# Kernel optimization log

Hardware: AMD Instinct MI355X
Metric: run time of the kernel (lower is better)

Reference implementation:

```python
import jax, jax.numpy as jnp
import numpy as np

B, NN, D, H, L, E, NC = 512, 64, 128, 4, 2, 262144, 8
N = B * NN
HD = D // H


def _mlp(x, W1, b1, W2, b2):
    return jax.nn.relu(x @ W1 + b1) @ W2 + b2


def setup_inputs() -> dict:
    key = jax.random.key(0)
    ks = iter(jax.random.split(key, 64))
    w = lambda shape, s=0.02: jax.random.normal(next(ks), shape, dtype=jnp.float32) * s
    inp = {
        'node_features': jax.random.randint(next(ks), (N,), 0, NC, dtype=jnp.int32),
        'edge_index': jax.random.randint(next(ks), (2, E), 0, N, dtype=jnp.int32),
        'ptr': jnp.arange(B + 1, dtype=jnp.int32) * NN,
        'node_emb_table': w((NC, D), 1.0),
        'edge_emb': jnp.clip(jax.random.normal(next(ks), (1, D), dtype=jnp.float32), -2.0, 2.0),
        'eW1': w((L, 3 * D, D)), 'eb1': jnp.zeros((L, D)), 'eW2': w((L, D, D)), 'eb2': jnp.zeros((L, D)),
        'nW1': w((L, 3 * D, D)), 'nb1': jnp.zeros((L, D)), 'nW2': w((L, D, D)), 'nb2': jnp.zeros((L, D)),
        'gW1': w((L, 3 * D, D)), 'gb1': jnp.zeros((L, D)), 'gW2': w((L, D, D)), 'gb2': jnp.zeros((L, D)),
        'projW': w((D, 3 * D)), 'projb': jnp.zeros((3 * D,)),
        'Wq': w((D, D)), 'Wk': w((D, D)), 'Wv': w((D, D)),
        'bq': jnp.zeros((D,)), 'bk': jnp.zeros((D,)), 'bv': jnp.zeros((D,)),
        'outW': w((D, D)), 'outb': jnp.zeros((D,)),
        'sW1': w((D, D)), 'sb1': jnp.zeros((D,)), 'sW2': w((D, D)), 'sb2': jnp.zeros((D,)),
        'rW1': w((D, D)), 'rb1': jnp.zeros((D,)), 'rW2': w((D, D)), 'rb2': jnp.zeros((D,)),
        'stW1': w((D, D)), 'stb1': jnp.zeros((D,)), 'stW2': w((D, 1)), 'stb2': jnp.zeros((1,)),
        'temperature': jnp.float32(1.0),
    }
    return inp


def reference(node_features, edge_index, ptr, node_emb_table, edge_emb,
              eW1, eb1, eW2, eb2, nW1, nb1, nW2, nb2, gW1, gb1, gW2, gb2,
              projW, projb, Wq, Wk, Wv, bq, bk, bv, outW, outb,
              sW1, sb1, sW2, sb2, rW1, rb1, rW2, rb2,
              stW1, stb1, stW2, stb2, temperature):
    n_graphs = ptr.shape[0] - 1                       # static
    batch_idx = jnp.repeat(jnp.arange(n_graphs), NN)  # uniform graphs of NN nodes
    node_embs = node_emb_table[node_features]         # [N, D]
    edge_embs = jnp.broadcast_to(edge_emb, (edge_index.shape[1], D))  # [E, D]
    g = jnp.zeros((n_graphs, D), node_embs.dtype)
    src, dst = edge_index[0], edge_index[1]
    for l in range(L):
        ein = jnp.concatenate([node_embs[src], node_embs[dst], edge_embs], -1)  # [E, 3D]
        edge_embs = edge_embs + _mlp(ein, eW1[l], eb1[l], eW2[l], eb2[l])
        node_aggr = jax.ops.segment_sum(edge_embs, dst, num_segments=N)         # [N, D]
        nin = jnp.concatenate([node_embs, node_aggr, g[batch_idx]], -1)
        node_embs = node_embs + _mlp(nin, nW1[l], nb1[l], nW2[l], nb2[l])
        eg = jax.ops.segment_sum(node_aggr, batch_idx, num_segments=n_graphs)
        ng = jax.ops.segment_sum(node_embs, batch_idx, num_segments=n_graphs)
        g = g + _mlp(jnp.concatenate([ng, eg, g], -1), gW1[l], gb1[l], gW2[l], gb2[l])
    # projection + self-attention over the NN nodes of each graph
    x = node_embs.reshape(n_graphs, NN, D) @ projW + projb   # [B, NN, 3D]
    q, k, v = jnp.split(x, 3, axis=-1)
    qh = (q @ Wq + bq).reshape(n_graphs, NN, H, HD)
    kh = (k @ Wk + bk).reshape(n_graphs, NN, H, HD)
    vh = (v @ Wv + bv).reshape(n_graphs, NN, H, HD)
    scores = jnp.einsum('bqhd,bkhd->bhqk', qh, kh) / jnp.sqrt(jnp.float32(HD))
    attn = jax.nn.softmax(scores, axis=-1)
    ctx = jnp.einsum('bhqk,bkhd->bqhd', attn, vh).reshape(n_graphs, NN, D)
    a = ctx @ outW + outb
    senders = _mlp(a, sW1, sb1, sW2, sb2)
    receivers = _mlp(a, rW1, rb1, rW2, rb2)
    edge_actions = jnp.einsum('bqd,bkd->bqk', senders, receivers).reshape(n_graphs, NN * NN)
    edge_actions = edge_actions / jax.nn.softplus(temperature)
    stop = _mlp(g, stW1, stb1, stW2, stb2)[:, 0]
    at = jnp.full((n_graphs, 3), -jnp.inf, dtype=edge_actions.dtype)
    at = at.at[:, 1].set(jax.nn.log_sigmoid(-stop))   # ADD_EDGE
    at = at.at[:, 2].set(jax.nn.log_sigmoid(stop))    # EXIT
    return (at, edge_actions)
```

## Files before the change

kernel.cpp:

```cpp
#include <hip/hip_runtime.h>
#include <hip/hip_bf16.h>
#include <cstdint>
#include <cstddef>

#define D_   128
#define NN_  64
#define B_   512
#define N_   32768
#define E_   262144

typedef float4 f4;
typedef _Float16 h16;
typedef __attribute__((ext_vector_type(8))) _Float16 h16x8;
typedef __attribute__((ext_vector_type(4))) float f32x4;

__device__ __forceinline__ f4 ld4(const float* p) { return *(const f4*)p; }
__device__ __forceinline__ void st4(float* p, f4 v) { *(f4*)p = v; }

__device__ __forceinline__ int swz(int row, int slot) {
  return row * 128 + ((slot ^ (row & 7)) << 3);
}
__device__ __forceinline__ h16x8 pk8(f4 a, f4 b) {
  h16x8 v;
  v[0]=(h16)a.x; v[1]=(h16)a.y; v[2]=(h16)a.z; v[3]=(h16)a.w;
  v[4]=(h16)b.x; v[5]=(h16)b.y; v[6]=(h16)b.z; v[7]=(h16)b.w;
  return v;
}
#define MFMA16(a,b,c) __builtin_amdgcn_mfma_f32_16x16x32_f16((a),(b),(c),0,0,0)

__device__ __forceinline__ void stage_a32(const float* __restrict__ A, h16* A_s, int r0, int tid) {
  int r = tid >> 2, q = tid & 3;
  const float* Ar = A + (size_t)(r0 + r) * 128 + q * 32;
#pragma unroll
  for (int i = 0; i < 4; ++i)
    *(h16x8*)&A_s[swz(r, q * 4 + i)] = pk8(ld4(Ar + i * 8), ld4(Ar + i * 8 + 4));
}
__device__ __forceinline__ void stage_a16(const h16* __restrict__ A, h16* A_s, int r0, int tid) {
  int r = tid >> 2, q = tid & 3;
  const h16* Ar = A + (size_t)(r0 + r) * 128 + q * 32;
#pragma unroll
  for (int i = 0; i < 4; ++i)
    *(h16x8*)&A_s[swz(r, q * 4 + i)] = *(const h16x8*)(Ar + i * 8);
}
__device__ __forceinline__ void bfrag_g(const h16* __restrict__ Bt, int n0, int lq, int lr, h16x8 bf[2][4]) {
#pragma unroll
  for (int nf = 0; nf < 2; ++nf) {
    const h16* row = Bt + (size_t)(n0 + nf * 16 + lr) * 128 + lq * 8;
#pragma unroll
    for (int ks = 0; ks < 4; ++ks)
      bf[nf][ks] = *(const h16x8*)(row + ks * 32);
  }
}
__device__ __forceinline__ void mfma8(const h16* A_s, h16x8 bf[2][4], f32x4 acc[4][2], int lq, int lr) {
#pragma unroll
  for (int mf = 0; mf < 4; ++mf)
#pragma unroll
    for (int ks = 0; ks < 4; ++ks) {
      h16x8 af = *(h16x8*)&A_s[swz(mf * 16 + lr, ks * 4 + lq)];
      acc[mf][0] = MFMA16(af, bf[0][ks], acc[mf][0]);
      acc[mf][1] = MFMA16(af, bf[1][ks], acc[mf][1]);
    }
}
__device__ __forceinline__ void zacc(f32x4 acc[4][2]) {
#pragma unroll
  for (int mf = 0; mf < 4; ++mf) { acc[mf][0] = (f32x4)0.f; acc[mf][1] = (f32x4)0.f; }
}

__global__ __launch_bounds__(256)
void k_embed(const int* __restrict__ nf, const float* __restrict__ tab, float* __restrict__ out) {
  int idx = blockIdx.x * 256 + threadIdx.x;
  int row = idx >> 5, q = idx & 31;
  st4(out + (size_t)row * D_ + q * 4, ld4(tab + (size_t)nf[row] * D_ + q * 4));
}

__global__ __launch_bounds__(256)
void k_zero_cnt(int* __restrict__ cnt) { cnt[blockIdx.x * 256 + threadIdx.x] = 0; }

__global__ __launch_bounds__(256)
void k_hist(const int* __restrict__ dst, int* __restrict__ cnt) {
  atomicAdd(&cnt[dst[blockIdx.x * 256 + threadIdx.x]], 1);
}

__global__ __launch_bounds__(256)
void k_scan(const int* __restrict__ cnt, int* __restrict__ base, int* __restrict__ cursor) {
  __shared__ int sums[256];
  __shared__ int offs[256];
  const int t = threadIdx.x;
  const int start = t * 128;
  int s = 0;
  for (int i = 0; i < 128; ++i) s += cnt[start + i];
  sums[t] = s;
  __syncthreads();
  if (t == 0) { int acc = 0; for (int i = 0; i < 256; ++i) { offs[i] = acc; acc += sums[i]; } }
  __syncthreads();
  int off = offs[t];
  for (int i = 0; i < 128; ++i) { base[start + i] = off; cursor[start + i] = off; off += cnt[start + i]; }
  if (t == 255) base[N_] = off;
}

__global__ __launch_bounds__(256)
void k_scatter(const int* __restrict__ dst, int* __restrict__ cursor, int* __restrict__ eid) {
  int e = blockIdx.x * 256 + threadIdx.x;
  int p = atomicAdd(&cursor[dst[e]], 1);
  eid[p] = e;
}

__global__ __launch_bounds__(256)
void k_aggr(const h16* __restrict__ edgeb, const int* __restrict__ csrB,
            float* __restrict__ aggr) {
  const int node = blockIdx.x * 4 + (threadIdx.x >> 6);
  const int d2 = (threadIdx.x & 63) * 2;
  const int b0 = csrB[node], b1 = csrB[node + 1];
  float s0 = 0.f, s1 = 0.f;
  for (int i = b0; i < b1; ++i) {
    const h16* p = edgeb + (size_t)i * 128 + d2;
    s0 += (float)p[0]; s1 += (float)p[1];
  }
  aggr[(size_t)node * 128 + d2 + 0] = s0;
  aggr[(size_t)node * 128 + d2 + 1] = s1;
}

struct TP { const float* p[32]; };
__global__ __launch_bounds__(256)
void k_w2t(TP tp, h16* __restrict__ dst) {
  __shared__ h16 w_s[128][132];
  const float* S = tp.p[blockIdx.x];
  h16* Dd = dst + (size_t)blockIdx.x * 16384;
  const int t = threadIdx.x, r = t >> 1, hf = t & 1;
  for (int i = 0; i < 64; i += 4) {
    f4 x = ld4(S + r * 128 + hf * 64 + i);
    w_s[r][hf*64+i+0] = (h16)x.x; w_s[r][hf*64+i+1] = (h16)x.y;
    w_s[r][hf*64+i+2] = (h16)x.z; w_s[r][hf*64+i+3] = (h16)x.w;
  }
  __syncthreads();
  for (int i8 = 0; i8 < 64; i8 += 8) {
    h16x8 v;
#pragma unroll
    for (int j = 0; j < 8; ++j) v[j] = w_s[hf*64 + i8 + j][r];
    *(h16x8*)(Dd + (size_t)r * 128 + hf * 64 + i8) = v;
  }
}

__global__ __launch_bounds__(256, 2)
void k_weff(const float* __restrict__ projW, const h16* __restrict__ wt_qkv,
            h16* __restrict__ wout) {
  __shared__ h16 A_s[64 * 128];
  const int i = blockIdx.x >> 1, half = blockIdx.x & 1;
  const int r0 = half * 64;
  const int tid = threadIdx.x;
  const int lane = tid & 63, w = tid >> 6;
  const int n0 = w * 32, lq = lane >> 4, lr = lane & 15;
  stage_a16(wt_qkv + (size_t)i * 16384, A_s, r0, tid);
  __syncthreads();
  h16x8 bf[2][4];
#pragma unroll
  for (int nf = 0; nf < 2; ++nf) {
    const int r = n0 + nf * 16 + lr;
    const float* prow = projW + (size_t)r * 384 + i * 128 + lq * 8;
#pragma unroll
    for (int ks = 0; ks < 4; ++ks)
      bf[nf][ks] = pk8(ld4(prow + ks * 32), ld4(prow + ks * 32 + 4));
  }
  f32x4 acc[4][2];
  zacc(acc);
  mfma8(A_s, bf, acc, lq, lr);
  h16* Wo = wout + (size_t)i * 16384;
#pragma unroll
  for (int nf = 0; nf < 2; ++nf) {
    const int r = n0 + nf * 16 + lr;
#pragma unroll
    for (int mf = 0; mf < 4; ++mf)
#pragma unroll
      for (int reg = 0; reg < 4; ++reg)
        Wo[(size_t)(r0 + mf * 16 + lq * 4 + reg) * 128 + r] = (h16)acc[mf][nf][reg];
  }
}

__global__ __launch_bounds__(256, 2)
void k_gemm3o(const float* __restrict__ A,
              const h16* __restrict__ B1, const h16* __restrict__ B2,
              const h16* __restrict__ B3,
              const float* __restrict__ bias,
              h16* __restrict__ O1, h16* __restrict__ O2, h16* __restrict__ O3) {
  __shared__ h16 A_s[64 * 128];
  const int tid = threadIdx.x;
  const int r0 = blockIdx.x * 64;
  const int lane = tid & 63, w = tid >> 6;
  const int n0 = w * 32, lq = lane >> 4, lr = lane & 15;
  stage_a32(A, A_s, r0, tid);
  __syncthreads();
  const h16* Bs[3] = {B1, B2, B3};
  h16*       Os[3] = {O1, O2, O3};
#pragma unroll
  for (int o = 0; o < 3; ++o) {
    if (!Bs[o]) break;
    h16x8 bf[2][4];
    f32x4 acc[4][2];
    bfrag_g(Bs[o], n0, lq, lr, bf);
    zacc(acc);
    mfma8(A_s, bf, acc, lq, lr);
#pragma unroll
    for (int nf = 0; nf < 2; ++nf) {
      const int col = n0 + nf * 16 + lr;
      const float bv = bias ? bias[o * 128 + col] : 0.f;
#pragma unroll
      for (int mf = 0; mf < 4; ++mf)
#pragma unroll
        for (int reg = 0; reg < 4; ++reg)
          Os[o][(size_t)(r0 + mf * 16 + lq * 4 + reg) * 128 + col] = (h16)(acc[mf][nf][reg] + bv);
    }
  }
}

__global__ __launch_bounds__(256, 2)
void k_mlp2(const float* __restrict__ A1, const float* __restrict__ A2,
            const float* __restrict__ A3,
            const h16* __restrict__ B1a, const h16* __restrict__ B1b,
            const h16* __restrict__ B1c,
            const float* __restrict__ bias1,
            const h16* __restrict__ B2, const float* __restrict__ bias2,
            const float* __restrict__ addC,
            float* __restrict__ C) {
  __shared__ h16 A_s[64 * 128];
  const int tid = threadIdx.x;
  const int r0 = blockIdx.x * 64;
  const int lane = tid & 63, w = tid >> 6;
  const int n0 = w * 32, lq = lane >> 4, lr = lane & 15;
  h16x8 bf[2][4];
  f32x4 acc[4][2];
  zacc(acc);
  stage_a32(A1, A_s, r0, tid);
  __syncthreads();
  bfrag_g(B1a, n0, lq, lr, bf);
  mfma8(A_s, bf, acc, lq, lr);
  if (A2) {
    __syncthreads();
    stage_a32(A2, A_s, r0, tid);
    __syncthreads();
    bfrag_g(B1b, n0, lq, lr, bf);
    mfma8(A_s, bf, acc, lq, lr);
  }
  if (A3) {
    __syncthreads();
    stage_a32(A3, A_s, r0, tid);
    __syncthreads();
    bfrag_g(B1c, n0, lq, lr, bf);
    mfma8(A_s, bf, acc, lq, lr);
  }
  __syncthreads();
#pragma unroll
  for (int nf = 0; nf < 2; ++nf) {
    const int col = n0 + nf * 16 + lr;
    const float b1v = bias1 ? bias1[col] : 0.f;
#pragma unroll
    for (int mf = 0; mf < 4; ++mf)
#pragma unroll
      for (int reg = 0; reg < 4; ++reg) {
        const int row = mf * 16 + lq * 4 + reg;
        A_s[swz(row, col >> 3) + (col & 7)] = (h16)fmaxf(acc[mf][nf][reg] + b1v, 0.f);
      }
  }
  __syncthreads();
  bfrag_g(B2, n0, lq, lr, bf);
  zacc(acc);
  mfma8(A_s, bf, acc, lq, lr);
#pragma unroll
  for (int nf = 0; nf < 2; ++nf) {
    const int col = n0 + nf * 16 + lr;
    const float b2v = bias2 ? bias2[col] : 0.f;
#pragma unroll
    for (int mf = 0; mf < 4; ++mf)
#pragma unroll
      for (int reg = 0; reg < 4; ++reg) {
        const int row = r0 + mf * 16 + lq * 4 + reg;
        float x = acc[mf][nf][reg] + b2v;
        if (addC) x += addC[(size_t)row * 128 + col];
        C[(size_t)row * 128 + col] = x;
      }
  }
}

__global__ __launch_bounds__(256, 2)
void k_nodemlp(float* __restrict__ node, const float* __restrict__ aggr,
               const float* __restrict__ gbuf,
               const h16* __restrict__ B1a, const h16* __restrict__ B1b,
               const float* __restrict__ nW1c, const float* __restrict__ nb1,
               const h16* __restrict__ B2, const float* __restrict__ nb2,
               float* __restrict__ ngb, float* __restrict__ egb) {
  __shared__ h16 A_s[64 * 128];
  __shared__ float gt_s[2][128];
  __shared__ float eg_s[2][128];
  const int tid = threadIdx.x, g = blockIdx.x, r0 = g * 64;
  const int lane = tid & 63, w = tid >> 6;
  const int n0 = w * 32, lq = lane >> 4, lr = lane & 15;
  h16x8 bf[2][4];
  f32x4 acc[4][2];
  zacc(acc);
  stage_a32(node, A_s, r0, tid);
  __syncthreads();
  bfrag_g(B1a, n0, lq, lr, bf);
  mfma8(A_s, bf, acc, lq, lr);
  {
    const int col = tid & 127, half = tid >> 7;
    float s = 0.f;
    const float* gb = gbuf + (size_t)g * 128;
    for (int j = half * 64; j < half * 64 + 64; ++j)
      s += gb[j] * nW1c[(size_t)j * 128 + col];
    gt_s[half][col] = s;
  }
  __syncthreads();
  stage_a32(aggr, A_s, r0, tid);
  __syncthreads();
  bfrag_g(B1b, n0, lq, lr, bf);
  mfma8(A_s, bf, acc, lq, lr);
  {
    const int col = tid & 127, half = tid >> 7;
    float s = 0.f;
    for (int r = half * 32; r < half * 32 + 32; ++r)
      s += aggr[((size_t)r0 + r) * 128 + col];
    eg_s[half][col] = s;
  }
  __syncthreads();
#pragma unroll
  for (int nf = 0; nf < 2; ++nf) {
    const int col = n0 + nf * 16 + lr;
    const float gt = gt_s[0][col] + gt_s[1][col] + nb1[col];
#pragma unroll
    for (int mf = 0; mf < 4; ++mf)
#pragma unroll
      for (int reg = 0; reg < 4; ++reg) {
        const int row = mf * 16 + lq * 4 + reg;
        A_s[swz(row, col >> 3) + (col & 7)] = (h16)fmaxf(acc[mf][nf][reg] + gt, 0.f);
      }
  }
  if (tid < 128) egb[(size_t)g * 128 + tid] = eg_s[0][tid] + eg_s[1][tid];
  __syncthreads();
  bfrag_g(B2, n0, lq, lr, bf);
  zacc(acc);
  mfma8(A_s, bf, acc, lq, lr);
#pragma unroll
  for (int nf = 0; nf < 2; ++nf) {
    const int col = n0 + nf * 16 + lr;
    const float b2v = nb2[col];
    float cs = 0.f;
#pragma unroll
    for (int mf = 0; mf < 4; ++mf)
#pragma unroll
      for (int reg = 0; reg < 4; ++reg) {
        const int row = r0 + mf * 16 + lq * 4 + reg;
        float x = acc[mf][nf][reg] + b2v + node[(size_t)row * 128 + col];
        node[(size_t)row * 128 + col] = x;
        cs += x;
      }
    cs += __shfl_xor(cs, 16);
    cs += __shfl_xor(cs, 32);
    if (lq == 0) ngb[(size_t)g * 128 + col] = cs;
  }
}

__global__ __launch_bounds__(256, 2)
void k_mlp2d(const float* __restrict__ A,
             const h16* __restrict__ B1a, const float* __restrict__ b1a,
             const h16* __restrict__ B2a, const float* __restrict__ b2a, h16* __restrict__ O1,
             const h16* __restrict__ B1b, const float* __restrict__ b1b,
             const h16* __restrict__ B2b, const float* __restrict__ b2b, h16* __restrict__ O2) {
  __shared__ h16 A_s[64 * 128];
  __shared__ h16 H_s[64 * 128];
  const int tid = threadIdx.x, r0 = blockIdx.x * 64;
  const int lane = tid & 63, w = tid >> 6;
  const int n0 = w * 32, lq = lane >> 4, lr = lane & 15;
  stage_a32(A, A_s, r0, tid);
  __syncthreads();
  const h16* W1[2] = {B1a, B1b};
  const h16* W2[2] = {B2a, B2b};
  const float* bb1[2] = {b1a, b1b};
  const float* bb2[2] = {b2a, b2b};
  h16* OO[2] = {O1, O2};
#pragma unroll
  for (int c = 0; c < 2; ++c) {
    h16x8 bf[2][4];
    f32x4 acc[4][2];
    bfrag_g(W1[c], n0, lq, lr, bf);
    zacc(acc);
    mfma8(A_s, bf, acc, lq, lr);
#pragma unroll
    for (int nf = 0; nf < 2; ++nf) {
      const int col = n0 + nf * 16 + lr;
      const float b1v = bb1[c][col];
#pragma unroll
      for (int mf = 0; mf < 4; ++mf)
#pragma unroll
        for (int reg = 0; reg < 4; ++reg) {
          const int row = mf * 16 + lq * 4 + reg;
          H_s[swz(row, col >> 3) + (col & 7)] = (h16)fmaxf(acc[mf][nf][reg] + b1v, 0.f);
        }
    }
    __syncthreads();
    bfrag_g(W2[c], n0, lq, lr, bf);
    zacc(acc);
    mfma8(H_s, bf, acc, lq, lr);
#pragma unroll
    for (int nf = 0; nf < 2; ++nf) {
      const int col = n0 + nf * 16 + lr;
      const float b2v = bb2[c][col];
#pragma unroll
      for (int mf = 0; mf < 4; ++mf)
#pragma unroll
        for (int reg = 0; reg < 4; ++reg)
          OO[c][(size_t)(r0 + mf * 16 + lq * 4 + reg) * 128 + col] = (h16)(acc[mf][nf][reg] + b2v);
    }
    __syncthreads();
  }
}

__global__ __launch_bounds__(128)
void k_hc0(const float* __restrict__ ee, const float* __restrict__ W1c,
           const float* __restrict__ b1, float* __restrict__ hc0) {
  int j = threadIdx.x;
  float s = b1[j];
  for (int d = 0; d < 128; ++d) s += ee[d] * W1c[d * 128 + j];
  hc0[j] = s;
}

__global__ __launch_bounds__(256, 2)
void k_edge0(const int* __restrict__ src, const int* __restrict__ dst,
             const int* __restrict__ eid,
             const h16* __restrict__ hs, const h16* __restrict__ hd,
             const float* __restrict__ hc0, const h16* __restrict__ Wt2,
             const float* __restrict__ eb2, const float* __restrict__ ee,
             h16* __restrict__ edgeb) {
  __shared__ h16 H_s[64 * 128];
  __shared__ int ss[64], sd[64];
  const int tid = threadIdx.x;
  const int e0 = blockIdx.x * 64;
  const int lane = tid & 63, w = tid >> 6;
  const int n0 = w * 32, lq = lane >> 4, lr = lane & 15;
  if (tid < 64) { int e = eid[e0 + tid]; ss[tid] = src[e]; sd[tid] = dst[e]; }
  __syncthreads();
  {
    int e = tid >> 2, q = tid & 3;
    const h16* ps = hs + (size_t)ss[e] * 128 + q * 32;
    const h16* pd = hd + (size_t)sd[e] * 128 + q * 32;
#pragma unroll
    for (int i = 0; i < 4; ++i) {
      h16x8 a = *(const h16x8*)(ps + i * 8);
      h16x8 b = *(const h16x8*)(pd + i * 8);
      f4 c0 = ld4(hc0 + q * 32 + i * 8), c1 = ld4(hc0 + q * 32 + i * 8 + 4);
      h16x8 v;
      v[0]=(h16)fmaxf((float)a[0]+(float)b[0]+c0.x,0.f); v[1]=(h16)fmaxf((float)a[1]+(float)b[1]+c0.y,0.f);
      v[2]=(h16)fmaxf((float)a[2]+(float)b[2]+c0.z,0.f); v[3]=(h16)fmaxf((float)a[3]+(float)b[3]+c0.w,0.f);
      v[4]=(h16)fmaxf((float)a[4]+(float)b[4]+c1.x,0.f); v[5]=(h16)fmaxf((float)a[5]+(float)b[5]+c1.y,0.f);
      v[6]=(h16)fmaxf((float)a[6]+(float)b[6]+c1.z,0.f); v[7]=(h16)fmaxf((float)a[7]+(float)b[7]+c1.w,0.f);
      *(h16x8*)&H_s[swz(e, q * 4 + i)] = v;
    }
  }
  __syncthreads();
  h16x8 bf[2][4];
  f32x4 acc[4][2];
  bfrag_g(Wt2, n0, lq, lr, bf);
  zacc(acc);
  mfma8(H_s, bf, acc, lq, lr);
  __syncthreads();
#pragma unroll
  for (int nf = 0; nf < 2; ++nf) {
    const int col = n0 + nf * 16 + lr;
    const float base = eb2[col] + ee[col];
#pragma unroll
    for (int mf = 0; mf < 4; ++mf)
#pragma unroll
      for (int reg = 0; reg < 4; ++reg) {
        const int row = mf * 16 + lq * 4 + reg;
        H_s[swz(row, col >> 3) + (col & 7)] = (h16)(acc[mf][nf][reg] + base);
      }
  }
  __syncthreads();
  {
    int r = tid >> 2, q = tid & 3;
#pragma unroll
    for (int i = 0; i < 4; ++i) {
      int slot = q * 4 + i;
      h16x8 v = *(const h16x8*)&H_s[swz(r, slot)];
      *(h16x8*)(edgeb + (size_t)(e0 + r) * 128 + slot * 8) = v;
    }
  }
}

__global__ __launch_bounds__(256, 2)
void k_edge1(const int* __restrict__ src, const int* __restrict__ dst,
             const int* __restrict__ eid,
             h16* __restrict__ edgeb,
             const h16* __restrict__ hs, const h16* __restrict__ hd,
             const h16* __restrict__ Wt1c, const float* __restrict__ b1,
             const h16* __restrict__ Wt2, const float* __restrict__ b2) {
  __shared__ h16 T_s[64 * 128];
  __shared__ h16 HS_s[64 * 128];
  __shared__ int ss[64], sd[64];
  const int tid = threadIdx.x;
  const int e0 = blockIdx.x * 64;
  const int lane = tid & 63, w = tid >> 6;
  const int n0 = w * 32, lq = lane >> 4, lr = lane & 15;
  if (tid < 64) { int e = eid[e0 + tid]; ss[tid] = src[e]; sd[tid] = dst[e]; }
  {
    int r = tid >> 2, q = tid & 3;
    const h16* Er = edgeb + (size_t)(e0 + r) * 128 + q * 32;
#pragma unroll
    for (int i = 0; i < 4; ++i)
      *(h16x8*)&T_s[swz(r, q * 4 + i)] = *(const h16x8*)(Er + i * 8);
  }
  __syncthreads();
  {
    int e = tid >> 2, q = tid & 3;
    const h16* ps = hs + (size_t)ss[e] * 128 + q * 32;
    const h16* pd = hd + (size_t)sd[e] * 128 + q * 32;
#pragma unroll
    for (int i = 0; i < 4; ++i) {
      h16x8 a = *(const h16x8*)(ps + i * 8);
      h16x8 b = *(const h16x8*)(pd + i * 8);
      f4 c0 = ld4(b1 + q * 32 + i * 8), c1 = ld4(b1 + q * 32 + i * 8 + 4);
      h16x8 v;
      v[0]=(h16)((float)a[0]+(float)b[0]+c0.x); v[1]=(h16)((float)a[1]+(float)b[1]+c0.y);
      v[2]=(h16)((float)a[2]+(float)b[2]+c0.z); v[3]=(h16)((float)a[3]+(float)b[3]+c0.w);
      v[4]=(h16)((float)a[4]+(float)b[4]+c1.x); v[5]=(h16)((float)a[5]+(float)b[5]+c1.y);
      v[6]=(h16)((float)a[6]+(float)b[6]+c1.z); v[7]=(h16)((float)a[7]+(float)b[7]+c1.w);
      *(h16x8*)&HS_s[swz(e, q * 4 + i)] = v;
    }
  }
  h16x8 bf[2][4];
  f32x4 acc[4][2];
  bfrag_g(Wt1c, n0, lq, lr, bf);
  zacc(acc);
  mfma8(T_s, bf, acc, lq, lr);
  float rres[2][4][4];
#pragma unroll
  for (int nf = 0; nf < 2; ++nf) {
    const int col = n0 + nf * 16 + lr;
#pragma unroll
    for (int mf = 0; mf < 4; ++mf)
#pragma unroll
      for (int reg = 0; reg < 4; ++reg) {
        const int row = mf * 16 + lq * 4 + reg;
        rres[nf][mf][reg] = (float)T_s[swz(row, col >> 3) + (col & 7)];
      }
  }
  __syncthreads();
#pragma unroll
  for (int nf = 0; nf < 2; ++nf) {
    const int col = n0 + nf * 16 + lr;
#pragma unroll
    for (int mf = 0; mf < 4; ++mf)
#pragma unroll
      for (int reg = 0; reg < 4; ++reg) {
        const int row = mf * 16 + lq * 4 + reg;
        float x = acc[mf][nf][reg] + (float)HS_s[swz(row, col >> 3) + (col & 7)];
        T_s[swz(row, col >> 3) + (col & 7)] = (h16)fmaxf(x, 0.f);
      }
  }
  __syncthreads();
  bfrag_g(Wt2, n0, lq, lr, bf);
  zacc(acc);
  mfma8(T_s, bf, acc, lq, lr);
#pragma unroll
  for (int nf = 0; nf < 2; ++nf) {
    const int col = n0 + nf * 16 + lr;
    const float b2v = b2[col];
#pragma unroll
    for (int mf = 0; mf < 4; ++mf)
#pragma unroll
      for (int reg = 0; reg < 4; ++reg) {
        const int row = mf * 16 + lq * 4 + reg;
        HS_s[swz(row, col >> 3) + (col & 7)] = (h16)(acc[mf][nf][reg] + b2v + rres[nf][mf][reg]);
      }
  }
  __syncthreads();
  {
    int r = tid >> 2, q = tid & 3;
#pragma unroll
    for (int i = 0; i < 4; ++i) {
      int slot = q * 4 + i;
      h16x8 v = *(const h16x8*)&HS_s[swz(r, slot)];
      *(h16x8*)(edgeb + (size_t)(e0 + r) * 128 + slot * 8) = v;
    }
  }
}

__global__ __launch_bounds__(128)
void k_beff(const float* __restrict__ projb,
            const float* __restrict__ Wq, const float* __restrict__ Wk, const float* __restrict__ Wv,
            const float* __restrict__ bq, const float* __restrict__ bk, const float* __restrict__ bv,
            float* __restrict__ beff) {
  int i = blockIdx.x, k = threadIdx.x;
  const float* W = (i == 0) ? Wq : ((i == 1) ? Wk : Wv);
  const float* bb = (i == 0) ? bq : ((i == 1) ? bk : bv);
  float s = bb[k];
  for (int j = 0; j < 128; ++j) s += projb[i * 128 + j] * W[j * 128 + k];
  beff[i * 128 + k] = s;
}

__global__ __launch_bounds__(256, 2)
void k_attn(const h16* __restrict__ Q, const h16* __restrict__ K,
            const h16* __restrict__ V, const h16* __restrict__ outWt,
            const float* __restrict__ outb, float* __restrict__ nodeOut) {
  __shared__ h16 k_s[64][136];
  __shared__ h16 v_s[64][136];
  __shared__ h16 A_s[64 * 128];
  const int tid = threadIdx.x, blk = blockIdx.x;
  const size_t base = (size_t)blk * 64 * 128;
  {
    int r = tid >> 2, q = tid & 3;
#pragma unroll
    for (int i = 0; i < 4; ++i) {
      *(h16x8*)&k_s[r][q * 32 + i * 8] = *(const h16x8*)(K + base + r * 128 + q * 32 + i * 8);
      *(h16x8*)&v_s[r][q * 32 + i * 8] = *(const h16x8*)(V + base + r * 128 + q * 32 + i * 8);
    }
  }
  __syncthreads();
  const int w = tid >> 6, lane = tid & 63, co = w * 32;
  h16x8 qv[4];
#pragma unroll
  for (int j = 0; j < 4; ++j)
    qv[j] = *(const h16x8*)(Q + base + (size_t)lane * 128 + co + j * 8);
  float s[64];
  const float scale = 0.17677669529663688f;
#pragma unroll 8
  for (int k = 0; k < 64; ++k) {
    float a = 0.f;
#pragma unroll
    for (int j = 0; j < 4; ++j) {
      h16x8 k8 = *(const h16x8*)&k_s[k][co + j * 8];
#pragma unroll
      for (int t = 0; t < 8; ++t) a += (float)qv[j][t] * (float)k8[t];
    }
    s[k] = a * scale;
  }
  float m = s[0];
#pragma unroll
  for (int k = 1; k < 64; ++k) m = fmaxf(m, s[k]);
  float sum = 0.f;
#pragma unroll
  for (int k = 0; k < 64; ++k) { s[k] = expf(s[k] - m); sum += s[k]; }
  const float inv = 1.f / sum;
  f4 cv[8];
#pragma unroll
  for (int jj = 0; jj < 8; ++jj) cv[jj] = make_float4(0.f, 0.f, 0.f, 0.f);
#pragma unroll 4
  for (int k = 0; k < 64; ++k) {
    float p = s[k];
#pragma unroll
    for (int j = 0; j < 4; ++j) {
      h16x8 v8 = *(const h16x8*)&v_s[k][co + j * 8];
      cv[2*j].x   += p * (float)v8[0]; cv[2*j].y   += p * (float)v8[1];
      cv[2*j].z   += p * (float)v8[2]; cv[2*j].w   += p * (float)v8[3];
      cv[2*j+1].x += p * (float)v8[4]; cv[2*j+1].y += p * (float)v8[5];
      cv[2*j+1].z += p * (float)v8[6]; cv[2*j+1].w += p * (float)v8[7];
    }
  }
#pragma unroll
  for (int jj = 0; jj < 4; ++jj) {
    f4 a = cv[2*jj], b = cv[2*jj+1];
    a.x *= inv; a.y *= inv; a.z *= inv; a.w *= inv;
    b.x *= inv; b.y *= inv; b.z *= inv; b.w *= inv;
    *(h16x8*)&A_s[swz(lane, (co >> 3) + jj)] = pk8(a, b);
  }
  __syncthreads();
  const int n0 = w * 32, lq = lane >> 4, lr = lane & 15;
  h16x8 bf[2][4];
  f32x4 acc[4][2];
  bfrag_g(outWt, n0, lq, lr, bf);
  zacc(acc);
  mfma8(A_s, bf, acc, lq, lr);
#pragma unroll
  for (int nf = 0; nf < 2; ++nf) {
    const int col = n0 + nf * 16 + lr;
    const float bv = outb[col];
#pragma unroll
    for (int mf = 0; mf < 4; ++mf)
#pragma unroll
      for (int reg = 0; reg < 4; ++reg)
        nodeOut[base + (size_t)(mf * 16 + lq * 4 + reg) * 128 + col] = acc[mf][nf][reg] + bv;
  }
}

__global__ __launch_bounds__(256, 2)
void k_edgeact(const h16* __restrict__ S, const h16* __restrict__ R,
               const float* __restrict__ temp, float* __restrict__ out) {
  __shared__ h16 S_s[64 * 128];
  const int tid = threadIdx.x;
  const int b = blockIdx.x;
  const size_t base = (size_t)b * 64 * 128;
  {
    int r = tid >> 2, q = tid & 3;
#pragma unroll
    for (int i = 0; i < 4; ++i)
      *(h16x8*)&S_s[swz(r, q * 4 + i)] = *(const h16x8*)(S + base + r * 128 + (q * 4 + i) * 8);
  }
  __syncthreads();
  const int lane = tid & 63, w = tid >> 6;
  const int n0 = w * 16, lq = lane >> 4, lr = lane & 15;
  h16x8 bf[4];
#pragma unroll
  for (int ks = 0; ks < 4; ++ks)
    bf[ks] = *(const h16x8*)(R + base + (size_t)(n0 + lr) * 128 + lq * 8 + ks * 32);
  f32x4 acc[4];
#pragma unroll
  for (int mf = 0; mf < 4; ++mf) acc[mf] = (f32x4)0.f;
#pragma unroll
  for (int mf = 0; mf < 4; ++mf)
#pragma unroll
    for (int ks = 0; ks < 4; ++ks) {
      h16x8 af = *(h16x8*)&S_s[swz(mf * 16 + lr, ks * 4 + lq)];
      acc[mf] = MFMA16(af, bf[ks], acc[mf]);
    }
  const float inv = 1.f / log1pf(expf(temp[0]));
  __syncthreads();
  float* O_s = (float*)S_s;
#pragma unroll
  for (int mf = 0; mf < 4; ++mf)
#pragma unroll
    for (int reg = 0; reg < 4; ++reg)
      O_s[(mf * 16 + lq * 4 + reg) * 64 + n0 + lr] = acc[mf][reg] * inv;
  __syncthreads();
#pragma unroll
  for (int i = 0; i < 4; ++i)
    st4(out + (size_t)b * 4096 + tid * 16 + i * 4, *(const f4*)&O_s[tid * 16 + i * 4]);
}

__global__ __launch_bounds__(256, 2)
void k_stophead(const float* __restrict__ gbuf, const h16* __restrict__ stW1t,
                const float* __restrict__ stb1, const float* __restrict__ stW2,
                const float* __restrict__ stb2, float* __restrict__ out) {
  __shared__ h16 A_s[64 * 128];
  __shared__ h16 H_s[64 * 128];
  const int tid = threadIdx.x, r0 = blockIdx.x * 64;
  const int lane = tid & 63, w = tid >> 6;
  const int n0 = w * 32, lq = lane >> 4, lr = lane & 15;
  stage_a32(gbuf, A_s, r0, tid);
  __syncthreads();
  h16x8 bf[2][4];
  f32x4 acc[4][2];
  bfrag_g(stW1t, n0, lq, lr, bf);
  zacc(acc);
  mfma8(A_s, bf, acc, lq, lr);
#pragma unroll
  for (int nf = 0; nf < 2; ++nf) {
    const int col = n0 + nf * 16 + lr;
    const float b1v = stb1[col];
#pragma unroll
    for (int mf = 0; mf < 4; ++mf)
#pragma unroll
      for (int reg = 0; reg < 4; ++reg) {
        const int row = mf * 16 + lq * 4 + reg;
        H_s[swz(row, col >> 3) + (col & 7)] = (h16)fmaxf(acc[mf][nf][reg] + b1v, 0.f);
      }
  }
  __syncthreads();
  if (tid < 64) {
    float s = stb2[0];
    for (int c = 0; c < 128; ++c)
      s += (float)H_s[swz(tid, c >> 3) + (c & 7)] * stW2[c];
    float l = log1pf(expf(-fabsf(s)));
    int b = r0 + tid;
    out[b * 3 + 0] = -3.3895313892515355e38f;
    out[b * 3 + 1] = fminf(-s, 0.f) - l;
    out[b * 3 + 2] = fminf(s, 0.f) - l;
  }
}

static const size_t OFF_NODE  = 0;
static const size_t OFF_HSRC  = 4194304;
static const size_t OFF_HDST  = 8388608;
static const size_t OFF_AGGR  = 12582912;
static const size_t OFF_HID   = 16777216;
static const size_t OFF_G     = 20971520;
static const size_t OFF_NG    = OFF_G + 65536;
static const size_t OFF_EG    = OFF_NG + 65536;
static const size_t OFF_BEFF  = OFF_EG + 65536;
static const size_t OFF_HC0   = OFF_BEFF + 384;
static const size_t OFF_EDGE  = 21495808;
static const size_t OFF_CSR   = OFF_EDGE + (size_t)E_ * 128;
static const size_t CSR_INTS  = (size_t)N_ + (N_ + 1) + N_ + E_;
static const size_t OFF_WT    = OFF_CSR + ((CSR_INTS + 63) & ~(size_t)63) / 1 / 4 * 4 + 64;

#define WT_WQ 0
#define WT_WK 1
#define WT_WV 2
#define WT_OUTW 3
#define WT_SW1 4
#define WT_SW2 5
#define WT_RW1 6
#define WT_RW2 7
#define WT_STW1 8
#define WT_L(l,i) (9 + (l)*11 + (i))
#define WT_EW1C1 31
#define WT_WEFF 32
#define WTP(i) (wt + (size_t)(i) * 16384)

extern "C" void kernel_launch(void* const* d_in, const int* in_sizes, int n_in,
                              void* d_out, int out_size, void* d_ws, size_t ws_size,
                              hipStream_t stream) {
  (void)in_sizes; (void)n_in; (void)out_size; (void)ws_size;
  const int*   nf    = (const int*)d_in[0];
  const int*   ei    = (const int*)d_in[1];
  const float* tab   = (const float*)d_in[3];
  const float* ee    = (const float*)d_in[4];
  const float* eW1   = (const float*)d_in[5];
  const float* eb1   = (const float*)d_in[6];
  const float* eW2   = (const float*)d_in[7];
  const float* eb2   = (const float*)d_in[8];
  const float* nW1   = (const float*)d_in[9];
  const float* nb1   = (const float*)d_in[10];
  const float* nW2   = (const float*)d_in[11];
  const float* nb2   = (const float*)d_in[12];
  const float* gW1   = (const float*)d_in[13];
  const float* gb1   = (const float*)d_in[14];
  const float* gW2   = (const float*)d_in[15];
  const float* gb2   = (const float*)d_in[16];
  const float* projW = (const float*)d_in[17];
  const float* projb = (const float*)d_in[18];
  const float* Wq    = (const float*)d_in[19];
  const float* Wk    = (const float*)d_in[20];
  const float* Wv    = (const float*)d_in[21];
  const float* bq    = (const float*)d_in[22];
  const float* bk    = (const float*)d_in[23];
  const float* bv    = (const float*)d_in[24];
  const float* outW  = (const float*)d_in[25];
  const float* outb  = (const float*)d_in[26];
  const float* sW1   = (const float*)d_in[27];
  const float* sb1   = (const float*)d_in[28];
  const float* sW2   = (const float*)d_in[29];
  const float* sb2   = (const float*)d_in[30];
  const float* rW1   = (const float*)d_in[31];
  const float* rb1   = (const float*)d_in[32];
  const float* rW2   = (const float*)d_in[33];
  const float* rb2   = (const float*)d_in[34];
  const float* stW1  = (const float*)d_in[35];
  const float* stb1  = (const float*)d_in[36];
  const float* stW2  = (const float*)d_in[37];
  const float* stb2  = (const float*)d_in[38];
  const float* temp  = (const float*)d_in[39];

  const int* srcI = ei;
  const int* dstI = ei + E_;

  float* ws    = (float*)d_ws;
  float* node  = ws + OFF_NODE;
  float* hsrcF = ws + OFF_HSRC;
  float* hdstF = ws + OFF_HDST;
  float* aggr  = ws + OFF_AGGR;
  float* hid   = ws + OFF_HID;
  float* gbuf  = ws + OFF_G;
  float* ngb   = ws + OFF_NG;
  float* egb   = ws + OFF_EG;
  float* beff  = ws + OFF_BEFF;
  float* hc0   = ws + OFF_HC0;
  h16*  hsrcH  = (h16*)hsrcF;
  h16*  hdstH  = (h16*)hdstF;
  h16*  vH     = (h16*)hid;
  h16*  edgebH = (h16*)(ws + OFF_EDGE);
  int* cnt    = (int*)(ws + OFF_CSR);
  int* csrB   = cnt + N_;
  int* cursor = csrB + (N_ + 1);
  int* eidL   = cursor + N_;
  h16* wt     = (h16*)(ws + OFF_WT);
  float* outp = (float*)d_out;

  hipMemsetAsync(gbuf, 0, (size_t)B_ * D_ * sizeof(float), stream);
  k_embed<<<4096, 256, 0, stream>>>(nf, tab, node);

  k_zero_cnt<<<N_ / 256, 256, 0, stream>>>(cnt);
  k_hist<<<E_ / 256, 256, 0, stream>>>(dstI, cnt);
  k_scan<<<1, 256, 0, stream>>>(cnt, csrB, cursor);
  k_scatter<<<E_ / 256, 256, 0, stream>>>(dstI, cursor, eidL);

  TP tp;
  tp.p[WT_WQ] = Wq; tp.p[WT_WK] = Wk; tp.p[WT_WV] = Wv; tp.p[WT_OUTW] = outW;
  tp.p[WT_SW1] = sW1; tp.p[WT_SW2] = sW2; tp.p[WT_RW1] = rW1; tp.p[WT_RW2] = rW2;
  tp.p[WT_STW1] = stW1;
  for (int l = 0; l < 2; ++l) {
    tp.p[WT_L(l,0)]  = eW1 + (size_t)l * 384 * 128;
    tp.p[WT_L(l,1)]  = eW1 + (size_t)l * 384 * 128 + 128 * 128;
    tp.p[WT_L(l,2)]  = eW2 + (size_t)l * 128 * 128;
    tp.p[WT_L(l,3)]  = nW1 + (size_t)l * 384 * 128;
    tp.p[WT_L(l,4)]  = nW1 + (size_t)l * 384 * 128 + 128 * 128;
    tp.p[WT_L(l,5)]  = nW1 + (size_t)l * 384 * 128 + 256 * 128;
    tp.p[WT_L(l,6)]  = nW2 + (size_t)l * 128 * 128;
    tp.p[WT_L(l,7)]  = gW1 + (size_t)l * 384 * 128;
    tp.p[WT_L(l,8)]  = gW1 + (size_t)l * 384 * 128 + 128 * 128;
    tp.p[WT_L(l,9)]  = gW1 + (size_t)l * 384 * 128 + 256 * 128;
    tp.p[WT_L(l,10)] = gW2 + (size_t)l * 128 * 128;
  }
  tp.p[WT_EW1C1] = eW1 + (size_t)384 * 128 + 256 * 128;
  k_w2t<<<32, 256, 0, stream>>>(tp, wt);

  k_weff<<<6, 256, 0, stream>>>(projW, WTP(WT_WQ), WTP(WT_WEFF));
  k_beff<<<3, 128, 0, stream>>>(projb, Wq, Wk, Wv, bq, bk, bv, beff);

  for (int l = 0; l < 2; ++l) {
    const float* eb1l = eb1 + l * 128;
    const float* eb2l = eb2 + l * 128;
    const float* nb1l = nb1 + l * 128;
    const float* nb2l = nb2 + l * 128;
    const float* gb1l = gb1 + l * 128;
    const float* gb2l = gb2 + l * 128;
    const float* nW1cl = nW1 + (size_t)l * 384 * 128 + 256 * 128;

    k_gemm3o<<<N_ / 64, 256, 0, stream>>>(node, WTP(WT_L(l,0)), WTP(WT_L(l,1)), nullptr,
                                          nullptr, hsrcH, hdstH, nullptr);
    if (l == 0) {
      k_hc0<<<1, 128, 0, stream>>>(ee, eW1 + 256 * 128, eb1l, hc0);
      k_edge0<<<E_ / 64, 256, 0, stream>>>(srcI, dstI, eidL, hsrcH, hdstH, hc0,
                                           WTP(WT_L(0,2)), eb2l, ee, edgebH);
    } else {
      k_edge1<<<E_ / 64, 256, 0, stream>>>(srcI, dstI, eidL, edgebH, hsrcH, hdstH,
                                           WTP(WT_EW1C1), eb1l, WTP(WT_L(1,2)), eb2l);
    }
    k_aggr<<<N_ / 4, 256, 0, stream>>>(edgebH, csrB, aggr);
    k_nodemlp<<<B_, 256, 0, stream>>>(node, aggr, gbuf,
                                      WTP(WT_L(l,3)), WTP(WT_L(l,4)),
                                      nW1cl, nb1l,
                                      WTP(WT_L(l,6)), nb2l, ngb, egb);
    k_mlp2<<<B_ / 64, 256, 0, stream>>>(ngb, egb, gbuf,
                                        WTP(WT_L(l,7)), WTP(WT_L(l,8)), WTP(WT_L(l,9)),
                                        gb1l,
                                        WTP(WT_L(l,10)), gb2l, gbuf, gbuf);
  }

  k_gemm3o<<<N_ / 64, 256, 0, stream>>>(node, WTP(WT_WEFF + 0), WTP(WT_WEFF + 1), WTP(WT_WEFF + 2),
                                        beff, hsrcH, hdstH, vH);
  k_attn<<<B_, 256, 0, stream>>>(hsrcH, hdstH, vH, WTP(WT_OUTW), outb, node);
  k_mlp2d<<<N_ / 64, 256, 0, stream>>>(node,
                                       WTP(WT_SW1), sb1, WTP(WT_SW2), sb2, hsrcH,
                                       WTP(WT_RW1), rb1, WTP(WT_RW2), rb2, hdstH);
  k_edgeact<<<B_, 256, 0, stream>>>(hsrcH, hdstH, temp, outp + 3 * B_);
  k_stophead<<<B_ / 64, 256, 0, stream>>>(gbuf, WTP(WT_STW1), stb1, stW2, stb2, outp);
}
```

Baseline: 451.5 us.

## Fuse QKV projection into attention and sender/receiver MLPs into edge-action kernel

The separate QKV GEMM kernel is folded into the attention kernel, so Q/K/V tiles are computed straight into shared memory per graph instead of round-tripping through global memory. The sender/receiver MLPs are fused into the edge-action kernel the same way, which removes two launches and the intermediate fp16 buffers. The edge kernels' launch bounds also rise from 2 to 4 blocks per CU, which may force register spills. The fused kernels use more shared memory per block (about 68 KB), which may limit occupancy.

Result: slower. 469.7 us (+4.0%).

```diff
diff --git a/kernel.cpp b/kernel.cpp
--- a/kernel.cpp
+++ b/kernel.cpp
@@ -358,61 +358,6 @@
   }
 }
 
-__global__ __launch_bounds__(256, 2)
-void k_mlp2d(const float* __restrict__ A,
-             const h16* __restrict__ B1a, const float* __restrict__ b1a,
-             const h16* __restrict__ B2a, const float* __restrict__ b2a, h16* __restrict__ O1,
-             const h16* __restrict__ B1b, const float* __restrict__ b1b,
-             const h16* __restrict__ B2b, const float* __restrict__ b2b, h16* __restrict__ O2) {
-  __shared__ h16 A_s[64 * 128];
-  __shared__ h16 H_s[64 * 128];
-  const int tid = threadIdx.x, r0 = blockIdx.x * 64;
-  const int lane = tid & 63, w = tid >> 6;
-  const int n0 = w * 32, lq = lane >> 4, lr = lane & 15;
-  stage_a32(A, A_s, r0, tid);
-  __syncthreads();
-  const h16* W1[2] = {B1a, B1b};
-  const h16* W2[2] = {B2a, B2b};
-  const float* bb1[2] = {b1a, b1b};
-  const float* bb2[2] = {b2a, b2b};
-  h16* OO[2] = {O1, O2};
-#pragma unroll
-  for (int c = 0; c < 2; ++c) {
-    h16x8 bf[2][4];
-    f32x4 acc[4][2];
-    bfrag_g(W1[c], n0, lq, lr, bf);
-    zacc(acc);
-    mfma8(A_s, bf, acc, lq, lr);
-#pragma unroll
-    for (int nf = 0; nf < 2; ++nf) {
-      const int col = n0 + nf * 16 + lr;
-      const float b1v = bb1[c][col];
-#pragma unroll
-      for (int mf = 0; mf < 4; ++mf)
-#pragma unroll
-        for (int reg = 0; reg < 4; ++reg) {
-          const int row = mf * 16 + lq * 4 + reg;
-          H_s[swz(row, col >> 3) + (col & 7)] = (h16)fmaxf(acc[mf][nf][reg] + b1v, 0.f);
-        }
-    }
-    __syncthreads();
-    bfrag_g(W2[c], n0, lq, lr, bf);
-    zacc(acc);
-    mfma8(H_s, bf, acc, lq, lr);
-#pragma unroll
-    for (int nf = 0; nf < 2; ++nf) {
-      const int col = n0 + nf * 16 + lr;
-      const float b2v = bb2[c][col];
-#pragma unroll
-      for (int mf = 0; mf < 4; ++mf)
-#pragma unroll
-        for (int reg = 0; reg < 4; ++reg)
-          OO[c][(size_t)(r0 + mf * 16 + lq * 4 + reg) * 128 + col] = (h16)(acc[mf][nf][reg] + b2v);
-    }
-    __syncthreads();
-  }
-}
-
 __global__ __launch_bounds__(128)
 void k_hc0(const float* __restrict__ ee, const float* __restrict__ W1c,
            const float* __restrict__ b1, float* __restrict__ hc0) {
@@ -422,7 +367,7 @@
   hc0[j] = s;
 }
 
-__global__ __launch_bounds__(256, 2)
+__global__ __launch_bounds__(256, 4)
 void k_edge0(const int* __restrict__ src, const int* __restrict__ dst,
              const int* __restrict__ eid,
              const h16* __restrict__ hs, const h16* __restrict__ hd,
@@ -485,7 +430,7 @@
   }
 }
 
-__global__ __launch_bounds__(256, 2)
+__global__ __launch_bounds__(256, 4)
 void k_edge1(const int* __restrict__ src, const int* __restrict__ dst,
              const int* __restrict__ eid,
              h16* __restrict__ edgeb,
@@ -597,28 +542,50 @@
 }
 
 __global__ __launch_bounds__(256, 2)
-void k_attn(const h16* __restrict__ Q, const h16* __restrict__ K,
-            const h16* __restrict__ V, const h16* __restrict__ outWt,
-            const float* __restrict__ outb, float* __restrict__ nodeOut) {
+void k_qkv_attn(const float* __restrict__ node_in,
+                const h16* __restrict__ Wq_t, const h16* __restrict__ Wk_t,
+                const h16* __restrict__ Wv_t, const float* __restrict__ beff,
+                const h16* __restrict__ outWt, const float* __restrict__ outb,
+                float* __restrict__ nodeOut) {
+  __shared__ h16 A_s[64 * 128];
+  __shared__ h16 q_s[64][136];
   __shared__ h16 k_s[64][136];
   __shared__ h16 v_s[64][136];
-  __shared__ h16 A_s[64 * 128];
-  const int tid = threadIdx.x, blk = blockIdx.x;
-  const size_t base = (size_t)blk * 64 * 128;
-  {
-    int r = tid >> 2, q = tid & 3;
-#pragma unroll
-    for (int i = 0; i < 4; ++i) {
-      *(h16x8*)&k_s[r][q * 32 + i * 8] = *(const h16x8*)(K + base + r * 128 + q * 32 + i * 8);
-      *(h16x8*)&v_s[r][q * 32 + i * 8] = *(const h16x8*)(V + base + r * 128 + q * 32 + i * 8);
-    }
-  }
-  __syncthreads();
-  const int w = tid >> 6, lane = tid & 63, co = w * 32;
+  const int tid = threadIdx.x, g = blockIdx.x, r0 = g * 64;
+  const int lane = tid & 63, w = tid >> 6;
+  const int n0 = w * 32, lq = lane >> 4, lr = lane & 15;
+  stage_a32(node_in, A_s, r0, tid);
+  __syncthreads();
+  const h16* Ws[3] = {Wq_t, Wk_t, Wv_t};
+#pragma unroll
+  for (int o = 0; o < 3; ++o) {
+    h16x8 bf[2][4];
+    f32x4 acc[4][2];
+    bfrag_g(Ws[o], n0, lq, lr, bf);
+    zacc(acc);
+    mfma8(A_s, bf, acc, lq, lr);
+#pragma unroll
+    for (int nf = 0; nf < 2; ++nf) {
+      const int col = n0 + nf * 16 + lr;
+      const float bv = beff[o * 128 + col];
+#pragma unroll
+      for (int mf = 0; mf < 4; ++mf)
+#pragma unroll
+        for (int reg = 0; reg < 4; ++reg) {
+          const int row = mf * 16 + lq * 4 + reg;
+          h16 x = (h16)(acc[mf][nf][reg] + bv);
+          if (o == 0) q_s[row][col] = x;
+          else if (o == 1) k_s[row][col] = x;
+          else v_s[row][col] = x;
+        }
+    }
+  }
+  __syncthreads();
+  const int co = n0;
   h16x8 qv[4];
 #pragma unroll
   for (int j = 0; j < 4; ++j)
-    qv[j] = *(const h16x8*)(Q + base + (size_t)lane * 128 + co + j * 8);
+    qv[j] = *(const h16x8*)&q_s[lane][co + j * 8];
   float s[64];
   const float scale = 0.17677669529663688f;
 #pragma unroll 8
@@ -662,12 +629,12 @@
     *(h16x8*)&A_s[swz(lane, (co >> 3) + jj)] = pk8(a, b);
   }
   __syncthreads();
-  const int n0 = w * 32, lq = lane >> 4, lr = lane & 15;
   h16x8 bf[2][4];
   f32x4 acc[4][2];
   bfrag_g(outWt, n0, lq, lr, bf);
   zacc(acc);
   mfma8(A_s, bf, acc, lq, lr);
+  const size_t base = (size_t)r0 * 128;
 #pragma unroll
   for (int nf = 0; nf < 2; ++nf) {
     const int col = n0 + nf * 16 + lr;
@@ -681,47 +648,114 @@
 }
 
 __global__ __launch_bounds__(256, 2)
-void k_edgeact(const h16* __restrict__ S, const h16* __restrict__ R,
-               const float* __restrict__ temp, float* __restrict__ out) {
+void k_sr_edgeact(const float* __restrict__ node_in,
+                  const h16* __restrict__ sW1t, const float* __restrict__ sb1,
+                  const h16* __restrict__ sW2t, const float* __restrict__ sb2,
+                  const h16* __restrict__ rW1t, const float* __restrict__ rb1,
+                  const h16* __restrict__ rW2t, const float* __restrict__ rb2,
+                  const float* __restrict__ temp, float* __restrict__ out) {
+  __shared__ h16 A_s[64 * 128];
+  __shared__ h16 H_s[64 * 128];
   __shared__ h16 S_s[64 * 128];
-  const int tid = threadIdx.x;
-  const int b = blockIdx.x;
-  const size_t base = (size_t)b * 64 * 128;
-  {
-    int r = tid >> 2, q = tid & 3;
-#pragma unroll
-    for (int i = 0; i < 4; ++i)
-      *(h16x8*)&S_s[swz(r, q * 4 + i)] = *(const h16x8*)(S + base + r * 128 + (q * 4 + i) * 8);
-  }
-  __syncthreads();
+  __shared__ h16 R_s[64][136];
+  const int tid = threadIdx.x, g = blockIdx.x, r0 = g * 64;
   const int lane = tid & 63, w = tid >> 6;
-  const int n0 = w * 16, lq = lane >> 4, lr = lane & 15;
-  h16x8 bf[4];
+  const int n0 = w * 32, lq = lane >> 4, lr = lane & 15;
+  stage_a32(node_in, A_s, r0, tid);
+  __syncthreads();
+  h16x8 bf[2][4];
+  f32x4 acc[4][2];
+  bfrag_g(sW1t, n0, lq, lr, bf);
+  zacc(acc);
+  mfma8(A_s, bf, acc, lq, lr);
+#pragma unroll
+  for (int nf = 0; nf < 2; ++nf) {
+    const int col = n0 + nf * 16 + lr;
+    const float b1v = sb1[col];
+#pragma unroll
+    for (int mf = 0; mf < 4; ++mf)
+#pragma unroll
+      for (int reg = 0; reg < 4; ++reg) {
+        const int row = mf * 16 + lq * 4 + reg;
+        H_s[swz(row, col >> 3) + (col & 7)] = (h16)fmaxf(acc[mf][nf][reg] + b1v, 0.f);
+      }
+  }
+  __syncthreads();
+  bfrag_g(sW2t, n0, lq, lr, bf);
+  zacc(acc);
+  mfma8(H_s, bf, acc, lq, lr);
+#pragma unroll
+  for (int nf = 0; nf < 2; ++nf) {
+    const int col = n0 + nf * 16 + lr;
+    const float b2v = sb2[col];
+#pragma unroll
+    for (int mf = 0; mf < 4; ++mf)
+#pragma unroll
+      for (int reg = 0; reg < 4; ++reg) {
+        const int row = mf * 16 + lq * 4 + reg;
+        S_s[swz(row, col >> 3) + (col & 7)] = (h16)(acc[mf][nf][reg] + b2v);
+      }
+  }
+  __syncthreads();
+  bfrag_g(rW1t, n0, lq, lr, bf);
+  zacc(acc);
+  mfma8(A_s, bf, acc, lq, lr);
+#pragma unroll
+  for (int nf = 0; nf < 2; ++nf) {
+    const int col = n0 + nf * 16 + lr;
+    const float b1v = rb1[col];
+#pragma unroll
+    for (int mf = 0; mf < 4; ++mf)
+#pragma unroll
+      for (int reg = 0; reg < 4; ++reg) {
+        const int row = mf * 16 + lq * 4 + reg;
+        H_s[swz(row, col >> 3) + (col & 7)] = (h16)fmaxf(acc[mf][nf][reg] + b1v, 0.f);
+      }
+  }
+  __syncthreads();
+  bfrag_g(rW2t, n0, lq, lr, bf);
+  zacc(acc);
+  mfma8(H_s, bf, acc, lq, lr);
+#pragma unroll
+  for (int nf = 0; nf < 2; ++nf) {
+    const int col = n0 + nf * 16 + lr;
+    const float b2v = rb2[col];
+#pragma unroll
+    for (int mf = 0; mf < 4; ++mf)
+#pragma unroll
+      for (int reg = 0; reg < 4; ++reg) {
+        const int row = mf * 16 + lq * 4 + reg;
+        R_s[row][col] = (h16)(acc[mf][nf][reg] + b2v);
+      }
+  }
+  __syncthreads();
+  const int n0e = w * 16;
+  h16x8 bfR[4];
 #pragma unroll
   for (int ks = 0; ks < 4; ++ks)
-    bf[ks] = *(const h16x8*)(R + base + (size_t)(n0 + lr) * 128 + lq * 8 + ks * 32);
-  f32x4 acc[4];
-#pragma unroll
-  for (int mf = 0; mf < 4; ++mf) acc[mf] = (f32x4)0.f;
+    bfR[ks] = *(const h16x8*)&R_s[n0e + lr][lq * 8 + ks * 32];
+  f32x4 acc4[4];
+#pragma unroll
+  for (int mf = 0; mf < 4; ++mf) acc4[mf] = (f32x4)0.f;
 #pragma unroll
   for (int mf = 0; mf < 4; ++mf)
 #pragma unroll
     for (int ks = 0; ks < 4; ++ks) {
       h16x8 af = *(h16x8*)&S_s[swz(mf * 16 + lr, ks * 4 + lq)];
-      acc[mf] = MFMA16(af, bf[ks], acc[mf]);
+      acc4[mf] = MFMA16(af, bfR[ks], acc4[mf]);
     }
   const float inv = 1.f / log1pf(expf(temp[0]));
   __syncthreads();
-  float* O_s = (float*)S_s;
+  float* O_s = (float*)H_s;
 #pragma unroll
   for (int mf = 0; mf < 4; ++mf)
 #pragma unroll
     for (int reg = 0; reg < 4; ++reg)
-      O_s[(mf * 16 + lq * 4 + reg) * 64 + n0 + lr] = acc[mf][reg] * inv;
+      O_s[(mf * 16 + lq * 4 + reg) * 64 + n0e + lr] = acc4[mf][reg] * inv;
   __syncthreads();
 #pragma unroll
   for (int i = 0; i < 4; ++i)
-    st4(out + (size_t)b * 4096 + tid * 16 + i * 4, *(const f4*)&O_s[tid * 16 + i * 4]);
+    st4(out + (size_t)g * 4096 + tid * 16 + i * 4, *(const f4*)&O_s[tid * 16 + i * 4]);
 }
 
 __global__ __launch_bounds__(256, 2)
@@ -769,7 +803,6 @@
 static const size_t OFF_HSRC  = 4194304;
 static const size_t OFF_HDST  = 8388608;
 static const size_t OFF_AGGR  = 12582912;
-static const size_t OFF_HID   = 16777216;
 static const size_t OFF_G     = 20971520;
 static const size_t OFF_NG    = OFF_G + 65536;
 static const size_t OFF_EG    = OFF_NG + 65536;
@@ -846,7 +879,6 @@
   float* hsrcF = ws + OFF_HSRC;
   float* hdstF = ws + OFF_HDST;
   float* aggr  = ws + OFF_AGGR;
-  float* hid   = ws + OFF_HID;
   float* gbuf  = ws + OFF_G;
   float* ngb   = ws + OFF_NG;
   float* egb   = ws + OFF_EG;
@@ -854,7 +886,6 @@
   float* hc0   = ws + OFF_HC0;
   h16*  hsrcH  = (h16*)hsrcF;
   h16*  hdstH  = (h16*)hdstF;
-  h16*  vH     = (h16*)hid;
   h16*  edgebH = (h16*)(ws + OFF_EDGE);
   int* cnt    = (int*)(ws + OFF_CSR);
   int* csrB   = cnt + N_;
@@ -924,12 +955,11 @@
                                         WTP(WT_L(l,10)), gb2l, gbuf, gbuf);
   }
 
-  k_gemm3o<<<N_ / 64, 256, 0, stream>>>(node, WTP(WT_WEFF + 0), WTP(WT_WEFF + 1), WTP(WT_WEFF + 2),
-                                        beff, hsrcH, hdstH, vH);
-  k_attn<<<B_, 256, 0, stream>>>(hsrcH, hdstH, vH, WTP(WT_OUTW), outb, node);
-  k_mlp2d<<<N_ / 64, 256, 0, stream>>>(node,
-                                       WTP(WT_SW1), sb1, WTP(WT_SW2), sb2, hsrcH,
-                                       WTP(WT_RW1), rb1, WTP(WT_RW2), rb2, hdstH);
-  k_edgeact<<<B_, 256, 0, stream>>>(hsrcH, hdstH, temp, outp + 3 * B_);
+  k_qkv_attn<<<B_, 256, 0, stream>>>(node, WTP(WT_WEFF + 0), WTP(WT_WEFF + 1),
+                                     WTP(WT_WEFF + 2), beff, WTP(WT_OUTW), outb, node);
+  k_sr_edgeact<<<B_, 256, 0, stream>>>(node,
+                                       WTP(WT_SW1), sb1, WTP(WT_SW2), sb2,
+                                       WTP(WT_RW1), rb1, WTP(WT_RW2), rb2,
+                                       temp, outp + 3 * B_);
   k_stophead<<<B_ / 64, 256, 0, stream>>>(gbuf, WTP(WT_STW1), stb1, stW2, stb2, outp);
 }
```
